# Kernel tuning notes

Measured on AMD Instinct MI355X. Metric: run time of the kernel, lower is better.

The kernel has to match this reference:

```python
import jax, jax.numpy as jnp
import numpy as np

B, N, DIM, HEADS, DIM_HEAD = 2, 2048, 1024, 16, 64
INNER = HEADS * DIM_HEAD
LN_EPS = 1e-5


def setup_inputs() -> dict:
    key = jax.random.key(0)
    k1, k2, k3 = jax.random.split(key, 3)
    x = jax.random.normal(k1, (B, N, DIM), dtype=jnp.float32)
    ln_w = jnp.ones((DIM,), dtype=jnp.float32)
    ln_b = jnp.zeros((DIM,), dtype=jnp.float32)
    w_qkv = jax.random.normal(k2, (DIM, 3 * INNER), dtype=jnp.float32) * (DIM ** -0.5)
    w_out = jax.random.normal(k3, (INNER, DIM), dtype=jnp.float32) * (INNER ** -0.5)
    return {"x": x, "ln_w": ln_w, "ln_b": ln_b, "w_qkv": w_qkv, "w_out": w_out}


def reference(x, ln_w, ln_b, w_qkv, w_out):
    scale = DIM_HEAD ** -0.5
    # LayerNorm over last dim
    mu = jnp.mean(x, axis=-1, keepdims=True)
    var = jnp.var(x, axis=-1, keepdims=True)
    xn = (x - mu) / jnp.sqrt(var + LN_EPS) * ln_w + ln_b
    # qkv projection, split, reshape to b h n d
    qkv = xn @ w_qkv  # [B, N, 3*INNER]
    q, k, v = jnp.split(qkv, 3, axis=-1)
    def to_heads(t):
        return t.reshape(B, N, HEADS, DIM_HEAD).transpose(0, 2, 1, 3)
    q, k, v = to_heads(q) * scale, to_heads(k), to_heads(v)
    # scores + causal mask (triu with offset 1 masked)
    sim = jnp.einsum('bhid,bhjd->bhij', q, k)  # [B, H, N, N]
    causal_mask = jnp.triu(jnp.ones((N, N), dtype=bool), k=1)
    sim = jnp.where(causal_mask, -jnp.finfo(sim.dtype).max, sim)
    attn = jax.nn.softmax(sim, axis=-1)
    out = jnp.einsum('bhij,bhjd->bhid', attn, v)  # [B, H, N, D]
    out = out.transpose(0, 2, 1, 3).reshape(B, N, INNER)
    return out @ w_out
```

## Files before the change

kernel.cpp:

```cpp
#include <hip/hip_runtime.h>
#include <stdint.h>

#define BATCH 2
#define NSEQ  2048
#define DIMC  1024
#define NHEAD 16
#define DHEAD 64
#define QKVN  3072
#define MROWS 4096

typedef __attribute__((ext_vector_type(8))) unsigned short u16x8;
typedef __attribute__((ext_vector_type(4))) unsigned short u16x4;
typedef __attribute__((ext_vector_type(8))) short          bf16x8;
typedef __attribute__((ext_vector_type(4))) float          f32x4;

#define F32_PROBE 0x3F800000u
#define QSCALE 0.18033688f

__device__ __forceinline__ float b2f(unsigned short u) {
  union { unsigned int i; float f; } c; c.i = ((unsigned int)u) << 16; return c.f;
}
__device__ __forceinline__ unsigned short f2b(float f) {
  unsigned int u = __float_as_uint(f);
  return (unsigned short)((u + 0x7fffu + ((u >> 16) & 1u)) >> 16);
}
__device__ __forceinline__ float fast_exp2(float x) {
  return __builtin_amdgcn_exp2f(x);
}
__device__ __forceinline__ void async16(const unsigned short* g, unsigned short* s) {
  __builtin_amdgcn_global_load_lds(
      (const __attribute__((address_space(1))) unsigned int*)g,
      (__attribute__((address_space(3))) unsigned int*)s, 16, 0, 0);
}

__device__ __forceinline__ void tr_tile(const void* __restrict__ in,
                                        unsigned short* __restrict__ out,
                                        int R, int C, int r0, int c0, bool f32,
                                        int t, unsigned short (*tile)[33],
                                        int scale_below) {
  int tx = t & 31, ty = t >> 5;
  float sc = (c0 < scale_below) ? QSCALE : 1.0f;
  if (f32) {
    #pragma unroll
    for (int i = 0; i < 32; i += 8)
      tile[ty + i][tx] = f2b(((const float*)in)[(size_t)(r0 + ty + i) * C + c0 + tx] * sc);
  } else {
    #pragma unroll
    for (int i = 0; i < 32; i += 8)
      tile[ty + i][tx] = f2b(b2f(((const unsigned short*)in)[(size_t)(r0 + ty + i) * C + c0 + tx]) * sc);
  }
  __syncthreads();
  #pragma unroll
  for (int i = 0; i < 32; i += 8)
    out[(size_t)(c0 + ty + i) * R + r0 + tx] = tile[tx][ty + i];
}

__global__ __launch_bounds__(256) void prep_kernel(const void* __restrict__ x,
                                                   const void* __restrict__ w,
                                                   const void* __restrict__ bb,
                                                   unsigned short* __restrict__ xn,
                                                   const void* __restrict__ w_qkv,
                                                   unsigned short* __restrict__ wqkvT,
                                                   const void* __restrict__ w_out,
                                                   unsigned short* __restrict__ woutT,
                                                   const unsigned int* __restrict__ probe) {
  __shared__ unsigned short tile[32][33];
  __shared__ float red[8];
  bool f32 = (*probe == F32_PROBE);
  int bid = blockIdx.x, t = threadIdx.x;

  if (bid < MROWS) {
    int row = bid;
    float v0, v1, v2, v3, w0, w1, w2, w3, bb0, bb1, bb2, bb3;
    if (f32) {
      const float* xr = (const float*)x + (size_t)row * DIMC;
      float4 xv = *(const float4*)(xr + t * 4);
      v0 = xv.x; v1 = xv.y; v2 = xv.z; v3 = xv.w;
      float4 wv = *(const float4*)((const float*)w + t * 4);
      w0 = wv.x; w1 = wv.y; w2 = wv.z; w3 = wv.w;
      float4 bv = *(const float4*)((const float*)bb + t * 4);
      bb0 = bv.x; bb1 = bv.y; bb2 = bv.z; bb3 = bv.w;
    } else {
      const unsigned short* xr = (const unsigned short*)x + (size_t)row * DIMC;
      u16x4 xv = *(const u16x4*)(xr + t * 4);
      v0 = b2f(xv[0]); v1 = b2f(xv[1]); v2 = b2f(xv[2]); v3 = b2f(xv[3]);
      u16x4 wv = *(const u16x4*)((const unsigned short*)w + t * 4);
      w0 = b2f(wv[0]); w1 = b2f(wv[1]); w2 = b2f(wv[2]); w3 = b2f(wv[3]);
      u16x4 bv = *(const u16x4*)((const unsigned short*)bb + t * 4);
      bb0 = b2f(bv[0]); bb1 = b2f(bv[1]); bb2 = b2f(bv[2]); bb3 = b2f(bv[3]);
    }
    float s = v0 + v1 + v2 + v3;
    float q = v0 * v0 + v1 * v1 + v2 * v2 + v3 * v3;
    #pragma unroll
    for (int off = 1; off < 64; off <<= 1) { s += __shfl_xor(s, off); q += __shfl_xor(q, off); }
    int wv_ = t >> 6;
    if ((t & 63) == 0) { red[wv_] = s; red[4 + wv_] = q; }
    __syncthreads();
    s = red[0] + red[1] + red[2] + red[3];
    q = red[4] + red[5] + red[6] + red[7];
    float mu  = s * (1.0f / DIMC);
    float var = q * (1.0f / DIMC) - mu * mu;
    float rstd = rsqrtf(var + 1e-5f);
    u16x4 o;
    o[0] = f2b((v0 - mu) * rstd * w0 + bb0);
    o[1] = f2b((v1 - mu) * rstd * w1 + bb1);
    o[2] = f2b((v2 - mu) * rstd * w2 + bb2);
    o[3] = f2b((v3 - mu) * rstd * w3 + bb3);
    *(u16x4*)(xn + (size_t)row * DIMC + t * 4) = o;
  } else if (bid < MROWS + 3072) {
    int tid = bid - MROWS;
    tr_tile(w_qkv, wqkvT, DIMC, QKVN, (tid / 96) * 32, (tid % 96) * 32, f32, t, tile, 1024);
  } else {
    int tid = bid - (MROWS + 3072);
    tr_tile(w_out, woutT, DIMC, DIMC, (tid >> 5) * 32, (tid & 31) * 32, f32, t, tile, 0);
  }
}

__global__ __launch_bounds__(256) void transpose_kernel(const void* __restrict__ in,
                                                        unsigned short* __restrict__ out,
                                                        int R, int C,
                                                        const unsigned int* __restrict__ probe) {
  __shared__ unsigned short tile[32][33];
  bool f32 = (*probe == F32_PROBE);
  int t = threadIdx.x;
  tr_tile(in, out, R, C, blockIdx.y * 32, blockIdx.x * 32, f32, t, tile, 0);
}

__global__ __launch_bounds__(256) void gemm_bt(const unsigned short* __restrict__ A,
                                               const unsigned short* __restrict__ Bt,
                                               void* __restrict__ Cv,
                                               int M, int N, int K, int lda,
                                               int detect_out,
                                               const unsigned int* __restrict__ probe,
                                               unsigned short* __restrict__ vt_out) {
  __shared__ unsigned short As[128 * 32];
  __shared__ unsigned short Bs[128 * 32];
  int t = threadIdx.x;
  int lane = t & 63, wave = t >> 6;
  int l16 = lane & 15, quad = lane >> 4;
  int wm = (wave & 1) * 64, wn = (wave >> 1) * 64;
  int bm = blockIdx.x * 128, bn = blockIdx.y * 128;

  f32x4 acc[4][4] = {};

  int srow = t >> 2;
  int scol = (t & 3) * 8;
  const unsigned short* Ap = A  + (size_t)(bm + srow) * lda + scol;
  const unsigned short* Bp = Bt + (size_t)(bn + srow) * K + scol;
  unsigned short* As0 = &As[srow * 32 + scol];
  unsigned short* As1 = &As[(64 + srow) * 32 + scol];
  unsigned short* Bs0 = &Bs[srow * 32 + scol];
  unsigned short* Bs1 = &Bs[(64 + srow) * 32 + scol];

  for (int k0 = 0; k0 < K; k0 += 32) {
    __syncthreads();
    async16(Ap + k0, As0);
    async16(Ap + (size_t)64 * lda + k0, As1);
    async16(Bp + k0, Bs0);
    async16(Bp + (size_t)64 * K + k0, Bs1);
    __syncthreads();
    bf16x8 af[4], bfr[4];
    #pragma unroll
    for (int mi = 0; mi < 4; mi++)
      af[mi] = *(const bf16x8*)&As[(wm + mi * 16 + l16) * 32 + quad * 8];
    #pragma unroll
    for (int ni = 0; ni < 4; ni++)
      bfr[ni] = *(const bf16x8*)&Bs[(wn + ni * 16 + l16) * 32 + quad * 8];
    #pragma unroll
    for (int mi = 0; mi < 4; mi++)
      #pragma unroll
      for (int ni = 0; ni < 4; ni++)
        acc[mi][ni] = __builtin_amdgcn_mfma_f32_16x16x32_bf16(af[mi], bfr[ni], acc[mi][ni], 0, 0, 0);
  }
  if (vt_out != nullptr && bn >= 2048) {
    #pragma unroll
    for (int mi = 0; mi < 4; mi++)
      #pragma unroll
      for (int ni = 0; ni < 4; ni++) {
        int gc = bn + wn + ni * 16 + l16;
        int hh = (gc >> 6) & 15;
        int dd = gc & 63;
        int gr0 = bm + wm + mi * 16 + quad * 4;
        int bb2 = gr0 >> 11;
        int n0  = gr0 & 2047;
        u16x4 pk;
        #pragma unroll
        for (int r = 0; r < 4; r++) pk[r] = f2b(acc[mi][ni][r]);
        *(u16x4*)&vt_out[(((size_t)(bb2 * 16 + hh) * 64 + dd) << 11) + n0] = pk;
      }
    return;
  }
  bool f32out = detect_out && (*probe == F32_PROBE);
  #pragma unroll
  for (int mi = 0; mi < 4; mi++)
    #pragma unroll
    for (int ni = 0; ni < 4; ni++)
      #pragma unroll
      for (int r = 0; r < 4; r++) {
        int gr = bm + wm + mi * 16 + quad * 4 + r;
        int gc = bn + wn + ni * 16 + l16;
        if (f32out) ((float*)Cv)[(size_t)gr * N + gc] = acc[mi][ni][r];
        else ((unsigned short*)Cv)[(size_t)gr * N + gc] = f2b(acc[mi][ni][r]);
      }
}

__global__ __launch_bounds__(256) void gemm_bt_n64(const unsigned short* __restrict__ A,
                                                   const unsigned short* __restrict__ Bt,
                                                   void* __restrict__ Cv,
                                                   int M, int N, int K, int lda,
                                                   int detect_out,
                                                   const unsigned int* __restrict__ probe) {
  __shared__ unsigned short As[128 * 32];
  __shared__ unsigned short Bs[64 * 32];
  int t = threadIdx.x;
  int lane = t & 63, wave = t >> 6;
  int l16 = lane & 15, quad = lane >> 4;
  int wm = (wave & 1) * 64, wn = (wave >> 1) * 32;
  int bm = blockIdx.x * 128, bn = blockIdx.y * 64;

  f32x4 acc[4][2] = {};

  int srow = t >> 2;
  int scol = (t & 3) * 8;
  const unsigned short* Ap = A  + (size_t)(bm + srow) * lda + scol;
  const unsigned short* Bp = Bt + (size_t)(bn + srow) * K + scol;
  unsigned short* As0 = &As[srow * 32 + scol];
  unsigned short* As1 = &As[(64 + srow) * 32 + scol];
  unsigned short* Bs0 = &Bs[srow * 32 + scol];

  for (int k0 = 0; k0 < K; k0 += 32) {
    __syncthreads();
    async16(Ap + k0, As0);
    async16(Ap + (size_t)64 * lda + k0, As1);
    async16(Bp + k0, Bs0);
    __syncthreads();
    bf16x8 af[4], bfr[2];
    #pragma unroll
    for (int mi = 0; mi < 4; mi++)
      af[mi] = *(const bf16x8*)&As[(wm + mi * 16 + l16) * 32 + quad * 8];
    #pragma unroll
    for (int ni = 0; ni < 2; ni++)
      bfr[ni] = *(const bf16x8*)&Bs[(wn + ni * 16 + l16) * 32 + quad * 8];
    #pragma unroll
    for (int mi = 0; mi < 4; mi++)
      #pragma unroll
      for (int ni = 0; ni < 2; ni++)
        acc[mi][ni] = __builtin_amdgcn_mfma_f32_16x16x32_bf16(af[mi], bfr[ni], acc[mi][ni], 0, 0, 0);
  }
  bool f32out = detect_out && (*probe == F32_PROBE);
  #pragma unroll
  for (int mi = 0; mi < 4; mi++)
    #pragma unroll
    for (int ni = 0; ni < 2; ni++)
      #pragma unroll
      for (int r = 0; r < 4; r++) {
        int gr = bm + wm + mi * 16 + quad * 4 + r;
        int gc = bn + wn + ni * 16 + l16;
        if (f32out) ((float*)Cv)[(size_t)gr * N + gc] = acc[mi][ni][r];
        else ((unsigned short*)Cv)[(size_t)gr * N + gc] = f2b(acc[mi][ni][r]);
      }
}

__device__ __forceinline__ int swz(int row, int chunk) {
  return row * 64 + ((chunk ^ (row & 7)) << 3);
}

__global__ __launch_bounds__(256) void attn_v4(unsigned short* __restrict__ qkv,
                                               const unsigned short* __restrict__ vt) {
  __shared__ unsigned short lds[20480];

  int t = threadIdx.x;
  int lane = t & 63, w = t >> 6;
  int l16 = lane & 15, quad = lane >> 4;
  int pair = blockIdx.x;
  int bh = blockIdx.y;
  int b = bh >> 4, h = bh & 15;
  unsigned short* qbase = qkv + (size_t)(b * NSEQ) * QKVN + h * DHEAD;
  const unsigned short* kbase = qbase + 1024;
  const unsigned short* vtb = vt + (size_t)bh * DHEAD * NSEQ;
  unsigned short* Ps = lds + 16384;

  int sr = t >> 3, sc = t & 7;

  for (int ph = 0; ph < 2; ph++) {
    int qt = ph ? pair : 31 - pair;
    int q0 = qt * 64;

    const unsigned short* qp = qbase + (size_t)(q0 + w * 16 + l16) * QKVN + quad * 8;
    bf16x8 bq0 = *(const bf16x8*)(qp);
    bf16x8 bq1 = *(const bf16x8*)(qp + 32);

    float l_i = 0.f;
    f32x4 o[4] = {};
    u16x8 k0r, k1r, v0r, v1r;

    if (ph) __syncthreads();

    k0r = *(const u16x8*)(kbase + (size_t)sr * QKVN + sc * 8);
    k1r = *(const u16x8*)(kbase + (size_t)(sr + 32) * QKVN + sc * 8);
    v0r = *(const u16x8*)(vtb + (size_t)sr * NSEQ + sc * 8);
    v1r = *(const u16x8*)(vtb + (size_t)(sr + 32) * NSEQ + sc * 8);
    *(u16x8*)&lds[swz(sr, sc)]             = k0r;
    *(u16x8*)&lds[swz(sr + 32, sc)]        = k1r;
    *(u16x8*)&lds[8192 + swz(sr, sc)]      = v0r;
    *(u16x8*)&lds[8192 + swz(sr + 32, sc)] = v1r;
    __syncthreads();

    for (int jt = 0; jt <= qt; jt++) {
      const unsigned short* Kc = lds + (jt & 1) * 4096;
      const unsigned short* Vc = lds + 8192 + (jt & 1) * 4096;

      if (jt < qt) {
        int j0n = (jt + 1) * 64;
        k0r = *(const u16x8*)(kbase + (size_t)(j0n + sr) * QKVN + sc * 8);
        k1r = *(const u16x8*)(kbase + (size_t)(j0n + sr + 32) * QKVN + sc * 8);
        v0r = *(const u16x8*)(vtb + (size_t)sr * NSEQ + j0n + sc * 8);
        v1r = *(const u16x8*)(vtb + (size_t)(sr + 32) * NSEQ + j0n + sc * 8);
      }

      f32x4 s[4];
      #pragma unroll
      for (int mj = 0; mj < 4; mj++)
        #pragma unroll
        for (int r = 0; r < 4; r++) s[mj][r] = -32.0f;
      #pragma unroll
      for (int mj = 0; mj < 4; mj++) {
        bf16x8 ak0 = *(const bf16x8*)&Kc[swz(mj * 16 + l16, quad)];
        s[mj] = __builtin_amdgcn_mfma_f32_16x16x32_bf16(ak0, bq0, s[mj], 0, 0, 0);
        bf16x8 ak1 = *(const bf16x8*)&Kc[swz(mj * 16 + l16, 4 + quad)];
        s[mj] = __builtin_amdgcn_mfma_f32_16x16x32_bf16(ak1, bq1, s[mj], 0, 0, 0);
      }

      if (jt == qt) {
        int il = w * 16 + l16;
        #pragma unroll
        for (int mj = 0; mj < 4; mj++)
          #pragma unroll
          for (int r = 0; r < 4; r++)
            if (mj * 16 + quad * 4 + r > il) s[mj][r] = -1e30f;
      }

      #pragma unroll
      for (int mj = 0; mj < 4; mj++) {
        u16x4 pk;
        #pragma unroll
        for (int r = 0; r < 4; r++) {
          float p = fast_exp2(s[mj][r]);
          l_i += p;
          pk[r] = f2b(p);
        }
        int ch = mj * 2 + (quad >> 1);
        *(u16x4*)&Ps[swz(w * 16 + l16, ch) + (quad & 1) * 4] = pk;
      }

      #pragma unroll
      for (int ks = 0; ks < 2; ks++) {
        bf16x8 ap = *(const bf16x8*)&Ps[swz(w * 16 + l16, ks * 4 + quad)];
        #pragma unroll
        for (int d = 0; d < 4; d++) {
          bf16x8 bv = *(const bf16x8*)&Vc[swz(d * 16 + l16, ks * 4 + quad)];
          o[d] = __builtin_amdgcn_mfma_f32_16x16x32_bf16(ap, bv, o[d], 0, 0, 0);
        }
      }

      if (jt < qt) {
        unsigned short* Kn = lds + ((jt + 1) & 1) * 4096;
        unsigned short* Vn = lds + 8192 + ((jt + 1) & 1) * 4096;
        *(u16x8*)&Kn[swz(sr, sc)]      = k0r;
        *(u16x8*)&Kn[swz(sr + 32, sc)] = k1r;
        *(u16x8*)&Vn[swz(sr, sc)]      = v0r;
        *(u16x8*)&Vn[swz(sr + 32, sc)] = v1r;
        __syncthreads();
      }
    }

    l_i += __shfl_xor(l_i, 16);
    l_i += __shfl_xor(l_i, 32);
    #pragma unroll
    for (int r = 0; r < 4; r++) {
      float lr = __shfl(l_i, (lane & 48) | (quad * 4 + r));
      float inv = 1.0f / lr;
      int row = q0 + w * 16 + quad * 4 + r;
      #pragma unroll
      for (int d = 0; d < 4; d++)
        qbase[(size_t)row * QKVN + d * 16 + l16] = f2b(o[d][r] * inv);
    }
  }
}

extern "C" void kernel_launch(void* const* d_in, const int* in_sizes, int n_in,
                              void* d_out, int out_size, void* d_ws, size_t ws_size,
                              hipStream_t stream) {
  const void* x     = d_in[0];
  const void* ln_w  = d_in[1];
  const void* ln_b  = d_in[2];
  const void* w_qkv = d_in[3];
  const void* w_out = d_in[4];
  const unsigned int* probe = (const unsigned int*)d_in[1];

  unsigned short* wqkvT = (unsigned short*)d_ws;
  unsigned short* qkv   = wqkvT + (size_t)QKVN * DIMC;
  unsigned short* xn    = (unsigned short*)d_out;
  size_t base_e  = (size_t)QKVN * DIMC + (size_t)MROWS * QKVN;
  size_t vt_e    = (size_t)BATCH * NHEAD * DHEAD * NSEQ;
  size_t wout_e  = (size_t)DIMC * DIMC;
  bool fit_vt  = ws_size >= (base_e + vt_e) * 2;
  bool fit_all = ws_size >= (base_e + vt_e + wout_e) * 2;
  unsigned short* vtp   = fit_vt ? qkv + (size_t)MROWS * QKVN
                                 : ((unsigned short*)d_out) + ((size_t)4 * 1024 * 1024);
  unsigned short* woutT = fit_all ? vtp + vt_e : wqkvT;

  int prep_blocks = MROWS + 3072 + (fit_all ? 1024 : 0);
  prep_kernel<<<prep_blocks, 256, 0, stream>>>(x, ln_w, ln_b, xn, w_qkv, wqkvT,
                                               w_out, fit_all ? woutT : nullptr, probe);
  gemm_bt<<<dim3(MROWS / 128, QKVN / 128), 256, 0, stream>>>(
      xn, wqkvT, qkv, MROWS, QKVN, DIMC, DIMC, 0, probe, vtp);
  if (!fit_all)
    transpose_kernel<<<dim3(DIMC / 32, DIMC / 32), 256, 0, stream>>>(w_out, woutT, DIMC, DIMC, probe);
  attn_v4<<<dim3(NSEQ / 128, BATCH * NHEAD), 256, 0, stream>>>(qkv, vtp);
  gemm_bt_n64<<<dim3(MROWS / 128, DIMC / 64), 256, 0, stream>>>(
      qkv, woutT, d_out, MROWS, DIMC, DIMC, QKVN, 1, probe);
}
```

Before: 185.5 us.

## Rewrite QKV GEMM with register-staged double-buffered LDS and swizzled layout

Replaces the QKV projection GEMM's single-buffered async LDS loads (two barriers per 32-wide K step) with a BK=64 double-buffered pipeline. The next tile is prefetched into registers during the MFMAs and stored to LDS using an XOR swizzle, leaving one barrier per step. The aim is to hide global-load latency, halve barrier count and avoid LDS bank conflicts. In exchange it uses more registers and twice the LDS, which may lower occupancy, and it specializes the kernel to fixed dimensions with bf16-only output.

```diff
diff --git a/kernel.cpp b/kernel.cpp
--- a/kernel.cpp
+++ b/kernel.cpp
@@ -31,6 +31,9 @@
   __builtin_amdgcn_global_load_lds(
       (const __attribute__((address_space(1))) unsigned int*)g,
       (__attribute__((address_space(3))) unsigned int*)s, 16, 0, 0);
+}
+__device__ __forceinline__ int swz(int row, int chunk) {
+  return row * 64 + ((chunk ^ (row & 7)) << 3);
 }
 
 __device__ __forceinline__ void tr_tile(const void* __restrict__ in,
@@ -126,15 +129,11 @@
   tr_tile(in, out, R, C, blockIdx.y * 32, blockIdx.x * 32, f32, t, tile, 0);
 }
 
-__global__ __launch_bounds__(256) void gemm_bt(const unsigned short* __restrict__ A,
-                                               const unsigned short* __restrict__ Bt,
-                                               void* __restrict__ Cv,
-                                               int M, int N, int K, int lda,
-                                               int detect_out,
-                                               const unsigned int* __restrict__ probe,
-                                               unsigned short* __restrict__ vt_out) {
-  __shared__ unsigned short As[128 * 32];
-  __shared__ unsigned short Bs[128 * 32];
+__global__ __launch_bounds__(256) void gemm1_v2(const unsigned short* __restrict__ A,
+                                                const unsigned short* __restrict__ Bt,
+                                                unsigned short* __restrict__ C,
+                                                unsigned short* __restrict__ vt_out) {
+  __shared__ unsigned short lds[32768];
   int t = threadIdx.x;
   int lane = t & 63, wave = t >> 6;
   int l16 = lane & 15, quad = lane >> 4;
@@ -143,36 +142,62 @@
 
   f32x4 acc[4][4] = {};
 
-  int srow = t >> 2;
-  int scol = (t & 3) * 8;
-  const unsigned short* Ap = A  + (size_t)(bm + srow) * lda + scol;
-  const unsigned short* Bp = Bt + (size_t)(bn + srow) * K + scol;
-  unsigned short* As0 = &As[srow * 32 + scol];
-  unsigned short* As1 = &As[(64 + srow) * 32 + scol];
-  unsigned short* Bs0 = &Bs[srow * 32 + scol];
-  unsigned short* Bs1 = &Bs[(64 + srow) * 32 + scol];
-
-  for (int k0 = 0; k0 < K; k0 += 32) {
-    __syncthreads();
-    async16(Ap + k0, As0);
-    async16(Ap + (size_t)64 * lda + k0, As1);
-    async16(Bp + k0, Bs0);
-    async16(Bp + (size_t)64 * K + k0, Bs1);
-    __syncthreads();
-    bf16x8 af[4], bfr[4];
-    #pragma unroll
-    for (int mi = 0; mi < 4; mi++)
-      af[mi] = *(const bf16x8*)&As[(wm + mi * 16 + l16) * 32 + quad * 8];
-    #pragma unroll
-    for (int ni = 0; ni < 4; ni++)
-      bfr[ni] = *(const bf16x8*)&Bs[(wn + ni * 16 + l16) * 32 + quad * 8];
-    #pragma unroll
-    for (int mi = 0; mi < 4; mi++)
+  int sr = t >> 3, sc = t & 7;
+  const unsigned short* Ap = A  + (size_t)(bm + sr) * DIMC + sc * 8;
+  const unsigned short* Bp = Bt + (size_t)(bn + sr) * DIMC + sc * 8;
+
+  u16x8 ar[4], br[4];
+  #pragma unroll
+  for (int i = 0; i < 4; i++) {
+    ar[i] = *(const u16x8*)(Ap + (size_t)i * 32 * DIMC);
+    br[i] = *(const u16x8*)(Bp + (size_t)i * 32 * DIMC);
+  }
+  #pragma unroll
+  for (int i = 0; i < 4; i++) {
+    *(u16x8*)&lds[swz(sr + i * 32, sc)]         = ar[i];
+    *(u16x8*)&lds[16384 + swz(sr + i * 32, sc)] = br[i];
+  }
+  __syncthreads();
+
+  for (int k = 0; k < 16; k++) {
+    if (k < 15) {
+      int c0 = (k + 1) * 64;
+      #pragma unroll
+      for (int i = 0; i < 4; i++) {
+        ar[i] = *(const u16x8*)(Ap + (size_t)i * 32 * DIMC + c0);
+        br[i] = *(const u16x8*)(Bp + (size_t)i * 32 * DIMC + c0);
+      }
+    }
+    const unsigned short* Ac = lds + (k & 1) * 8192;
+    const unsigned short* Bc = lds + 16384 + (k & 1) * 8192;
+    #pragma unroll
+    for (int ks = 0; ks < 2; ks++) {
+      bf16x8 af[4], bfr[4];
+      #pragma unroll
+      for (int mi = 0; mi < 4; mi++)
+        af[mi] = *(const bf16x8*)&Ac[swz(wm + mi * 16 + l16, ks * 4 + quad)];
       #pragma unroll
       for (int ni = 0; ni < 4; ni++)
-        acc[mi][ni] = __builtin_amdgcn_mfma_f32_16x16x32_bf16(af[mi], bfr[ni], acc[mi][ni], 0, 0, 0);
-  }
-  if (vt_out != nullptr && bn >= 2048) {
+        bfr[ni] = *(const bf16x8*)&Bc[swz(wn + ni * 16 + l16, ks * 4 + quad)];
+      #pragma unroll
+      for (int mi = 0; mi < 4; mi++)
+        #pragma unroll
+        for (int ni = 0; ni < 4; ni++)
+          acc[mi][ni] = __builtin_amdgcn_mfma_f32_16x16x32_bf16(af[mi], bfr[ni], acc[mi][ni], 0, 0, 0);
+    }
+    if (k < 15) {
+      unsigned short* An = lds + ((k + 1) & 1) * 8192;
+      unsigned short* Bn = lds + 16384 + ((k + 1) & 1) * 8192;
+      #pragma unroll
+      for (int i = 0; i < 4; i++) {
+        *(u16x8*)&An[swz(sr + i * 32, sc)] = ar[i];
+        *(u16x8*)&Bn[swz(sr + i * 32, sc)] = br[i];
+      }
+      __syncthreads();
+    }
+  }
+
+  if (bn >= 2048) {
     #pragma unroll
     for (int mi = 0; mi < 4; mi++)
       #pragma unroll
@@ -190,7 +215,6 @@
       }
     return;
   }
-  bool f32out = detect_out && (*probe == F32_PROBE);
   #pragma unroll
   for (int mi = 0; mi < 4; mi++)
     #pragma unroll
@@ -199,8 +223,7 @@
       for (int r = 0; r < 4; r++) {
         int gr = bm + wm + mi * 16 + quad * 4 + r;
         int gc = bn + wn + ni * 16 + l16;
-        if (f32out) ((float*)Cv)[(size_t)gr * N + gc] = acc[mi][ni][r];
-        else ((unsigned short*)Cv)[(size_t)gr * N + gc] = f2b(acc[mi][ni][r]);
+        C[(size_t)gr * QKVN + gc] = f2b(acc[mi][ni][r]);
       }
 }
 
@@ -261,10 +284,6 @@
       }
 }
 
-__device__ __forceinline__ int swz(int row, int chunk) {
-  return row * 64 + ((chunk ^ (row & 7)) << 3);
-}
-
 __global__ __launch_bounds__(256) void attn_v4(unsigned short* __restrict__ qkv,
                                                const unsigned short* __restrict__ vt) {
   __shared__ unsigned short lds[20480];
@@ -413,8 +432,7 @@
   int prep_blocks = MROWS + 3072 + (fit_all ? 1024 : 0);
   prep_kernel<<<prep_blocks, 256, 0, stream>>>(x, ln_w, ln_b, xn, w_qkv, wqkvT,
                                                w_out, fit_all ? woutT : nullptr, probe);
-  gemm_bt<<<dim3(MROWS / 128, QKVN / 128), 256, 0, stream>>>(
-      xn, wqkvT, qkv, MROWS, QKVN, DIMC, DIMC, 0, probe, vtp);
+  gemm1_v2<<<dim3(MROWS / 128, QKVN / 128), 256, 0, stream>>>(xn, wqkvT, qkv, vtp);
   if (!fit_all)
     transpose_kernel<<<dim3(DIMC / 32, DIMC / 32), 256, 0, stream>>>(w_out, woutT, DIMC, DIMC, probe);
   attn_v4<<<dim3(NSEQ / 128, BATCH * NHEAD), 256, 0, stream>>>(qkv, vtp);
```

Result: no change. 187.2 us (+0.9%).
